# Kernel tuning notes

Hardware: AMD Instinct MI355X
Metric: run time of the kernel (lower is better)

## Reference

```python
import jax, jax.numpy as jnp
import numpy as np

H, E, R = 1024, 48, 32  # hidden size, num entities, num relation types
MAX_START = 200


def setup_inputs() -> dict:
    key = jax.random.key(0)
    ks = jax.random.split(key, 6)
    return {
        "entity_emb": jax.random.normal(ks[0], (E, H), jnp.float32),
        "rel_emb": jax.random.normal(ks[1], (R, H), jnp.float32),
        "W1": jax.random.normal(ks[2], (3 * H, H), jnp.float32) / np.sqrt(3 * H).astype(np.float32),
        "b1": jnp.zeros((H,), jnp.float32),
        "W2": jax.random.normal(ks[3], (H, 1), jnp.float32) / np.sqrt(H).astype(np.float32),
        "b2": jnp.zeros((1,), jnp.float32),
        "entity_starts": jax.random.randint(ks[4], (E,), 0, MAX_START, jnp.int32),
        "max_distance": 50,
    }


def reference(entity_emb, rel_emb, W1, b1, W2, b2, entity_starts, max_distance):
    """Vectorized equivalent of the triple loop: for every (subj i, obj j, rel k)
    score = sigmoid(MLP(cat([subj, rel, obj]))), masked by i != j and
    |start_i - start_j| <= max_distance. Dropout is identity at eval."""
    e, h = entity_emb.shape
    r = rel_emb.shape[0]
    # build all triplet inputs [E, E, R, 3H] (cat order: subject, relation, object)
    s = jnp.broadcast_to(entity_emb[:, None, None, :], (e, e, r, h))
    rel = jnp.broadcast_to(rel_emb[None, None, :, :], (e, e, r, h))
    o = jnp.broadcast_to(entity_emb[None, :, None, :], (e, e, r, h))
    trip = jnp.concatenate([s, rel, o], axis=-1)  # [E, E, R, 3H]
    hid = jax.nn.relu(jnp.einsum("sorf,fh->sorh", trip, W1) + b1)  # [E, E, R, H]
    logits = jnp.einsum("sorh,hx->sorx", hid, W2)[..., 0] + b2[0]  # [E, E, R]
    scores = jax.nn.sigmoid(logits)
    # pair mask: no self-relations, distance cutoff
    dist = jnp.abs(entity_starts[:, None] - entity_starts[None, :])
    mask = (dist <= max_distance) & (~jnp.eye(e, dtype=bool))  # [E, E]
    return jnp.where(mask[:, :, None], scores, jnp.zeros((), scores.dtype))
```

## Files before the change

kernel.cpp:

```cpp
#include <hip/hip_runtime.h>
#include <hip/hip_bf16.h>
#include <math.h>

#define Hh 1024
#define Ee 48
#define Rr 32
#define PITCH_A 1028
#define PITCH_B 516

union F4 { float4 v; float f[4]; };

__global__ __launch_bounds__(512) void kA_table(const float* __restrict__ ent,
                                                const float* __restrict__ rel,
                                                const float* __restrict__ W1,
                                                const float* __restrict__ b1,
                                                float* __restrict__ T) {
    __shared__ float se[16 * PITCH_A];
    const int tid = threadIdx.x;
    const int rt = blockIdx.x & 7;
    const int h0 = (blockIdx.x >> 3) * 32;
    const int row0 = rt * 16;

    const float* emb; int foff;
    if (row0 < 48)      { emb = ent + row0 * Hh;        foff = 0;      }
    else if (row0 < 80) { emb = rel + (row0 - 48) * Hh; foff = Hh;     }
    else                { emb = ent + (row0 - 80) * Hh; foff = 2 * Hh; }

    for (int q = 0; q < 8; ++q) {
        const int id4 = tid + q * 512;
        const int r = id4 >> 8, o4 = id4 & 255;
        *reinterpret_cast<float4*>(&se[r * PITCH_A + o4 * 4]) =
            *reinterpret_cast<const float4*>(&emb[r * Hh + o4 * 4]);
    }
    __syncthreads();

    const int w    = tid >> 6;
    const int lane = tid & 63;
    const int h4g  = lane & 7;
    const int rsub = lane >> 3;
    const int r0 = rsub * 2, r1 = r0 + 1;
    const int fb = w * 128;

    const float* w1p = W1 + (size_t)(foff + fb) * Hh + h0 + h4g * 4;
    const float* e0p = se + r0 * PITCH_A + fb;
    const float* e1p = se + r1 * PITCH_A + fb;

    float acc[2][4];
#pragma unroll
    for (int a = 0; a < 2; ++a)
#pragma unroll
        for (int c = 0; c < 4; ++c) acc[a][c] = 0.f;

    F4 wk[4];
#pragma unroll
    for (int c = 0; c < 4; ++c)
        wk[c].v = *reinterpret_cast<const float4*>(w1p + (size_t)c * Hh);

    for (int s = 0; s < 32; ++s) {
        const int f = s * 4;
        F4 wn[4];
        if (s < 31) {
#pragma unroll
            for (int c = 0; c < 4; ++c)
                wn[c].v = *reinterpret_cast<const float4*>(w1p + (size_t)(f + 4 + c) * Hh);
        }
        F4 e0, e1;
        e0.v = *reinterpret_cast<const float4*>(e0p + f);
        e1.v = *reinterpret_cast<const float4*>(e1p + f);
#pragma unroll
        for (int c = 0; c < 4; ++c) {
#pragma unroll
            for (int hh = 0; hh < 4; ++hh) {
                acc[0][hh] = fmaf(e0.f[c], wk[c].f[hh], acc[0][hh]);
                acc[1][hh] = fmaf(e1.f[c], wk[c].f[hh], acc[1][hh]);
            }
        }
        if (s < 31) {
#pragma unroll
            for (int c = 0; c < 4; ++c) wk[c] = wn[c];
        }
    }

    __syncthreads();
    {
        float* part = se;
        const int base = (w * 64 + lane) * 8;
        F4 o0, o1;
#pragma unroll
        for (int c = 0; c < 4; ++c) { o0.f[c] = acc[0][c]; o1.f[c] = acc[1][c]; }
        *reinterpret_cast<float4*>(&part[base])     = o0.v;
        *reinterpret_cast<float4*>(&part[base + 4]) = o1.v;
    }
    __syncthreads();
    {
        const int r = tid >> 5, h = tid & 31;
        const int src = ((r >> 1) * 8 + (h >> 2)) * 8 + (r & 1) * 4 + (h & 3);
        float s = 0.f;
#pragma unroll
        for (int ww = 0; ww < 8; ++ww) s += se[ww * 512 + src];
        const int row = row0 + r;
        if (row >= 48 && row < 80) s += b1[h0 + h];
        T[row * Hh + h0 + h] = s;
    }
}

__global__ __launch_bounds__(512) void kB_triplets(const float* __restrict__ T,
                                                   const float* __restrict__ W2,
                                                   const float* __restrict__ b2,
                                                   const int* __restrict__ starts,
                                                   const int* __restrict__ maxd,
                                                   float* __restrict__ out) {
    __shared__ float se[42 * PITCH_B];
    const int tid = threadIdx.x;
    const int i  = blockIdx.x >> 2;
    const int js = (blockIdx.x >> 1) & 1;
    const int ks = blockIdx.x & 1;
    const int j0 = js * 24;
    const int k0 = ks * 16;

    const int w    = tid >> 6;
    const int lane = tid & 63;
    const int jG = lane & 7;
    const int kG = lane >> 3;

    float acc[3][2];
#pragma unroll
    for (int a = 0; a < 3; ++a) { acc[a][0] = 0.f; acc[a][1] = 0.f; }

    for (int c = 0; c < 2; ++c) {
        const int hbase = c * 512;
        __syncthreads();
        for (int q = 0; q < 11; ++q) {
            const int id4 = tid + q * 512;
            if (id4 < 5376) {
                const int g = id4 >> 7, o4 = id4 & 127;
                const float* src;
                if (g == 41) src = W2 + hbase + o4 * 4;
                else {
                    int grow;
                    if (g == 0)       grow = i;
                    else if (g < 17)  grow = 48 + k0 + (g - 1);
                    else              grow = 80 + j0 + (g - 17);
                    src = T + grow * Hh + hbase + o4 * 4;
                }
                *reinterpret_cast<float4*>(&se[g * PITCH_B + o4 * 4]) =
                    *reinterpret_cast<const float4*>(src);
            }
        }
        __syncthreads();

        const int hw = w * 64;
        const float* pa = se + hw;
        const float* pw = se + 41 * PITCH_B + hw;

#pragma unroll
        for (int s = 0; s < 16; ++s) {
            const int h4 = s * 4;
            F4 av, wv, rv[2], bv[3];
            av.v = *reinterpret_cast<const float4*>(pa + h4);
            wv.v = *reinterpret_cast<const float4*>(pw + h4);
#pragma unroll
            for (int tk = 0; tk < 2; ++tk)
                rv[tk].v = *reinterpret_cast<const float4*>(se + (1 + kG + 8 * tk) * PITCH_B + hw + h4);
#pragma unroll
            for (int tj = 0; tj < 3; ++tj)
                bv[tj].v = *reinterpret_cast<const float4*>(se + (17 + jG + 8 * tj) * PITCH_B + hw + h4);

#pragma unroll
            for (int cc = 0; cc < 4; ++cc) {
                const float a = av.f[cc], w2v = wv.f[cc];
                const float p0 = a + rv[0].f[cc];
                const float p1 = a + rv[1].f[cc];
#pragma unroll
                for (int tj = 0; tj < 3; ++tj) {
                    const float bb = bv[tj].f[cc];
                    float v0 = p0 + bb; v0 = v0 > 0.f ? v0 : 0.f;
                    acc[tj][0] = fmaf(v0, w2v, acc[tj][0]);
                    float v1 = p1 + bb; v1 = v1 > 0.f ? v1 : 0.f;
                    acc[tj][1] = fmaf(v1, w2v, acc[tj][1]);
                }
            }
        }
    }

    __syncthreads();
    {
        float* part = se;
#pragma unroll
        for (int tj = 0; tj < 3; ++tj)
#pragma unroll
            for (int tk = 0; tk < 2; ++tk)
                part[w * 384 + (tj * 8 + jG) * 16 + tk * 8 + kG] = acc[tj][tk];
    }
    __syncthreads();
    if (tid < 384) {
        float s = b2[0];
#pragma unroll
        for (int ww = 0; ww < 8; ++ww) s += se[ww * 384 + tid];
        const int jl = tid >> 4, kl = tid & 15;
        const int j = j0 + jl, k = k0 + kl;
        const float sc = 1.f / (1.f + expf(-s));
        int di = starts[i] - starts[j]; if (di < 0) di = -di;
        const bool m = (i != j) && (di <= maxd[0]);
        out[(i * Ee + j) * Rr + k] = m ? sc : 0.f;
    }
}

extern "C" void kernel_launch(void* const* d_in, const int* in_sizes, int n_in,
                              void* d_out, int out_size, void* d_ws, size_t ws_size,
                              hipStream_t stream) {
    const float* ent    = (const float*)d_in[0];
    const float* rel    = (const float*)d_in[1];
    const float* W1     = (const float*)d_in[2];
    const float* b1     = (const float*)d_in[3];
    const float* W2     = (const float*)d_in[4];
    const float* b2     = (const float*)d_in[5];
    const int*   starts = (const int*)d_in[6];
    const int*   maxd   = (const int*)d_in[7];
    float* out = (float*)d_out;

    float* T = (float*)d_ws;

    kA_table<<<256, 512, 0, stream>>>(ent, rel, W1, b1, T);
    kB_triplets<<<192, 512, 0, stream>>>(T, W2, b2, starts, maxd, out);
}
```

Baseline: 29.34 us.

## Double-buffer W1 and T tiles through LDS in both kernels

The table kernel now stages W1 in 256-row chunks into a double-buffered shared-memory tile, transposed so each h-group reads contiguous weights, instead of streaming W1 from global memory straight into registers. The triplet kernel splits the hidden dimension into four 256-wide chunks with ping-pong LDS buffers, so the global loads for the next chunk are issued before computing on the current one. The goal is to overlap global loads with FMA work and hide latency. In exchange, LDS use grows (kA goes to about 130KB), which may limit occupancy, and there are more barriers.

```diff
diff --git a/kernel.cpp b/kernel.cpp
--- a/kernel.cpp
+++ b/kernel.cpp
@@ -6,7 +6,10 @@
 #define Ee 48
 #define Rr 32
 #define PITCH_A 1028
-#define PITCH_B 516
+#define GP_A 1028
+#define BKa 256
+#define PITCH_B 260
+#define CH_B 256
 
 union F4 { float4 v; float f[4]; };
 
@@ -15,7 +18,8 @@
                                                 const float* __restrict__ W1,
                                                 const float* __restrict__ b1,
                                                 float* __restrict__ T) {
-    __shared__ float se[16 * PITCH_A];
+    __shared__ float emb_s[16 * PITCH_A];
+    __shared__ float w_s[2][8 * GP_A];
     const int tid = threadIdx.x;
     const int rt = blockIdx.x & 7;
     const int h0 = (blockIdx.x >> 3) * 32;
@@ -29,67 +33,70 @@
     for (int q = 0; q < 8; ++q) {
         const int id4 = tid + q * 512;
         const int r = id4 >> 8, o4 = id4 & 255;
-        *reinterpret_cast<float4*>(&se[r * PITCH_A + o4 * 4]) =
+        *reinterpret_cast<float4*>(&emb_s[r * PITCH_A + o4 * 4]) =
             *reinterpret_cast<const float4*>(&emb[r * Hh + o4 * 4]);
     }
-    __syncthreads();
 
     const int w    = tid >> 6;
     const int lane = tid & 63;
     const int h4g  = lane & 7;
     const int rsub = lane >> 3;
-    const int r0 = rsub * 2, r1 = r0 + 1;
-    const int fb = w * 128;
-
-    const float* w1p = W1 + (size_t)(foff + fb) * Hh + h0 + h4g * 4;
-    const float* e0p = se + r0 * PITCH_A + fb;
-    const float* e1p = se + r1 * PITCH_A + fb;
-
-    float acc[2][4];
-#pragma unroll
-    for (int a = 0; a < 2; ++a)
-#pragma unroll
-        for (int c = 0; c < 4; ++c) acc[a][c] = 0.f;
-
-    F4 wk[4];
-#pragma unroll
-    for (int c = 0; c < 4; ++c)
-        wk[c].v = *reinterpret_cast<const float4*>(w1p + (size_t)c * Hh);
-
-    for (int s = 0; s < 32; ++s) {
-        const int f = s * 4;
-        F4 wn[4];
-        if (s < 31) {
-#pragma unroll
-            for (int c = 0; c < 4; ++c)
-                wn[c].v = *reinterpret_cast<const float4*>(w1p + (size_t)(f + 4 + c) * Hh);
-        }
-        F4 e0, e1;
-        e0.v = *reinterpret_cast<const float4*>(e0p + f);
-        e1.v = *reinterpret_cast<const float4*>(e1p + f);
-#pragma unroll
-        for (int c = 0; c < 4; ++c) {
-#pragma unroll
-            for (int hh = 0; hh < 4; ++hh) {
-                acc[0][hh] = fmaf(e0.f[c], wk[c].f[hh], acc[0][hh]);
-                acc[1][hh] = fmaf(e1.f[c], wk[c].f[hh], acc[1][hh]);
+    const int r0 = rsub * 2;
+
+    const int sc4 = tid & 7;
+    const int sfb = tid >> 3;
+    auto stage = [&](int buf, int c) {
+        const float* gp = &W1[(size_t)(foff + c * BKa + sfb) * Hh + h0 + sc4 * 4];
+        float4 v0 = *reinterpret_cast<const float4*>(gp);
+        float4 v1 = *reinterpret_cast<const float4*>(gp + (size_t)64 * Hh);
+        float4 v2 = *reinterpret_cast<const float4*>(gp + (size_t)128 * Hh);
+        float4 v3 = *reinterpret_cast<const float4*>(gp + (size_t)192 * Hh);
+        float* lp = &w_s[buf][sc4 * GP_A + sfb * 4];
+        *reinterpret_cast<float4*>(lp)       = v0;
+        *reinterpret_cast<float4*>(lp + 256) = v1;
+        *reinterpret_cast<float4*>(lp + 512) = v2;
+        *reinterpret_cast<float4*>(lp + 768) = v3;
+    };
+
+    stage(0, 0);
+    __syncthreads();
+
+    float acc0[4] = {0.f, 0.f, 0.f, 0.f};
+    float acc1[4] = {0.f, 0.f, 0.f, 0.f};
+
+    for (int c = 0; c < 4; ++c) {
+        if (c < 3) stage((c + 1) & 1, c + 1);
+
+        const float* wp  = &w_s[c & 1][h4g * GP_A + (w * 32) * 4];
+        const float* e0p = &emb_s[r0 * PITCH_A + c * BKa + w * 32];
+        const float* e1p = e0p + PITCH_A;
+
+#pragma unroll
+        for (int s = 0; s < 8; ++s) {
+            F4 e0, e1;
+            e0.v = *reinterpret_cast<const float4*>(e0p + s * 4);
+            e1.v = *reinterpret_cast<const float4*>(e1p + s * 4);
+#pragma unroll
+            for (int ff = 0; ff < 4; ++ff) {
+                F4 wv;
+                wv.v = *reinterpret_cast<const float4*>(wp + (s * 4 + ff) * 4);
+#pragma unroll
+                for (int hh = 0; hh < 4; ++hh) {
+                    acc0[hh] = fmaf(e0.f[ff], wv.f[hh], acc0[hh]);
+                    acc1[hh] = fmaf(e1.f[ff], wv.f[hh], acc1[hh]);
+                }
             }
         }
-        if (s < 31) {
-#pragma unroll
-            for (int c = 0; c < 4; ++c) wk[c] = wn[c];
-        }
-    }
-
-    __syncthreads();
+        __syncthreads();
+    }
+
     {
-        float* part = se;
         const int base = (w * 64 + lane) * 8;
         F4 o0, o1;
 #pragma unroll
-        for (int c = 0; c < 4; ++c) { o0.f[c] = acc[0][c]; o1.f[c] = acc[1][c]; }
-        *reinterpret_cast<float4*>(&part[base])     = o0.v;
-        *reinterpret_cast<float4*>(&part[base + 4]) = o1.v;
+        for (int c = 0; c < 4; ++c) { o0.f[c] = acc0[c]; o1.f[c] = acc1[c]; }
+        *reinterpret_cast<float4*>(&emb_s[base])     = o0.v;
+        *reinterpret_cast<float4*>(&emb_s[base + 4]) = o1.v;
     }
     __syncthreads();
     {
@@ -97,7 +104,7 @@
         const int src = ((r >> 1) * 8 + (h >> 2)) * 8 + (r & 1) * 4 + (h & 3);
         float s = 0.f;
 #pragma unroll
-        for (int ww = 0; ww < 8; ++ww) s += se[ww * 512 + src];
+        for (int ww = 0; ww < 8; ++ww) s += emb_s[ww * 512 + src];
         const int row = row0 + r;
         if (row >= 48 && row < 80) s += b1[h0 + h];
         T[row * Hh + h0 + h] = s;
@@ -110,7 +117,7 @@
                                                    const int* __restrict__ starts,
                                                    const int* __restrict__ maxd,
                                                    float* __restrict__ out) {
-    __shared__ float se[42 * PITCH_B];
+    __shared__ float se[2][42 * PITCH_B];
     const int tid = threadIdx.x;
     const int i  = blockIdx.x >> 2;
     const int js = (blockIdx.x >> 1) & 1;
@@ -123,48 +130,69 @@
     const int jG = lane & 7;
     const int kG = lane >> 3;
 
+    auto stage = [&](int buf, int c) {
+        const int hbase = c * CH_B;
+        float4 v0, v1, v2, v3, v4, v5;
+        int a5 = -1;
+#define SRC_OF(ID4, VV)                                                       \
+        {                                                                     \
+            const int g = (ID4) >> 6, o4 = (ID4) & 63;                        \
+            const float* src;                                                 \
+            if (g == 41) src = W2 + hbase + o4 * 4;                           \
+            else {                                                            \
+                int grow;                                                     \
+                if (g == 0)       grow = i;                                   \
+                else if (g < 17)  grow = 48 + k0 + (g - 1);                   \
+                else              grow = 80 + j0 + (g - 17);                  \
+                src = T + grow * Hh + hbase + o4 * 4;                         \
+            }                                                                 \
+            VV = *reinterpret_cast<const float4*>(src);                       \
+        }
+        SRC_OF(tid,          v0)
+        SRC_OF(tid + 512,    v1)
+        SRC_OF(tid + 1024,   v2)
+        SRC_OF(tid + 1536,   v3)
+        SRC_OF(tid + 2048,   v4)
+        if (tid < 128) { SRC_OF(tid + 2560, v5) a5 = tid + 2560; }
+#undef SRC_OF
+        float* b = se[buf];
+        {
+            const int id4 = tid;        *reinterpret_cast<float4*>(&b[(id4 >> 6) * PITCH_B + (id4 & 63) * 4]) = v0;
+        }
+        { const int id4 = tid + 512;    *reinterpret_cast<float4*>(&b[(id4 >> 6) * PITCH_B + (id4 & 63) * 4]) = v1; }
+        { const int id4 = tid + 1024;   *reinterpret_cast<float4*>(&b[(id4 >> 6) * PITCH_B + (id4 & 63) * 4]) = v2; }
+        { const int id4 = tid + 1536;   *reinterpret_cast<float4*>(&b[(id4 >> 6) * PITCH_B + (id4 & 63) * 4]) = v3; }
+        { const int id4 = tid + 2048;   *reinterpret_cast<float4*>(&b[(id4 >> 6) * PITCH_B + (id4 & 63) * 4]) = v4; }
+        if (a5 >= 0) { *reinterpret_cast<float4*>(&b[(a5 >> 6) * PITCH_B + (a5 & 63) * 4]) = v5; }
+    };
+
+    stage(0, 0);
+    __syncthreads();
+
     float acc[3][2];
 #pragma unroll
     for (int a = 0; a < 3; ++a) { acc[a][0] = 0.f; acc[a][1] = 0.f; }
 
-    for (int c = 0; c < 2; ++c) {
-        const int hbase = c * 512;
-        __syncthreads();
-        for (int q = 0; q < 11; ++q) {
-            const int id4 = tid + q * 512;
-            if (id4 < 5376) {
-                const int g = id4 >> 7, o4 = id4 & 127;
-                const float* src;
-                if (g == 41) src = W2 + hbase + o4 * 4;
-                else {
-                    int grow;
-                    if (g == 0)       grow = i;
-                    else if (g < 17)  grow = 48 + k0 + (g - 1);
-                    else              grow = 80 + j0 + (g - 17);
-                    src = T + grow * Hh + hbase + o4 * 4;
-                }
-                *reinterpret_cast<float4*>(&se[g * PITCH_B + o4 * 4]) =
-                    *reinterpret_cast<const float4*>(src);
-            }
-        }
-        __syncthreads();
-
-        const int hw = w * 64;
-        const float* pa = se + hw;
-        const float* pw = se + 41 * PITCH_B + hw;
-
-#pragma unroll
-        for (int s = 0; s < 16; ++s) {
+    for (int c = 0; c < 4; ++c) {
+        if (c < 3) stage((c + 1) & 1, c + 1);
+
+        const float* sm = se[c & 1];
+        const int hw = w * 32;
+        const float* pa = sm + hw;
+        const float* pw = sm + 41 * PITCH_B + hw;
+
+#pragma unroll
+        for (int s = 0; s < 8; ++s) {
             const int h4 = s * 4;
             F4 av, wv, rv[2], bv[3];
             av.v = *reinterpret_cast<const float4*>(pa + h4);
             wv.v = *reinterpret_cast<const float4*>(pw + h4);
 #pragma unroll
             for (int tk = 0; tk < 2; ++tk)
-                rv[tk].v = *reinterpret_cast<const float4*>(se + (1 + kG + 8 * tk) * PITCH_B + hw + h4);
+                rv[tk].v = *reinterpret_cast<const float4*>(sm + (1 + kG + 8 * tk) * PITCH_B + hw + h4);
 #pragma unroll
             for (int tj = 0; tj < 3; ++tj)
-                bv[tj].v = *reinterpret_cast<const float4*>(se + (17 + jG + 8 * tj) * PITCH_B + hw + h4);
+                bv[tj].v = *reinterpret_cast<const float4*>(sm + (17 + jG + 8 * tj) * PITCH_B + hw + h4);
 
 #pragma unroll
             for (int cc = 0; cc < 4; ++cc) {
@@ -181,22 +209,19 @@
                 }
             }
         }
-    }
-
-    __syncthreads();
-    {
-        float* part = se;
-#pragma unroll
-        for (int tj = 0; tj < 3; ++tj)
-#pragma unroll
-            for (int tk = 0; tk < 2; ++tk)
-                part[w * 384 + (tj * 8 + jG) * 16 + tk * 8 + kG] = acc[tj][tk];
-    }
+        __syncthreads();
+    }
+
+#pragma unroll
+    for (int tj = 0; tj < 3; ++tj)
+#pragma unroll
+        for (int tk = 0; tk < 2; ++tk)
+            se[0][w * 384 + (tj * 8 + jG) * 16 + tk * 8 + kG] = acc[tj][tk];
     __syncthreads();
     if (tid < 384) {
         float s = b2[0];
 #pragma unroll
-        for (int ww = 0; ww < 8; ++ww) s += se[ww * 384 + tid];
+        for (int ww = 0; ww < 8; ++ww) s += se[0][ww * 384 + tid];
         const int jl = tid >> 4, kl = tid & 15;
         const int j = j0 + jl, k = k0 + kl;
         const float sc = 1.f / (1.f + expf(-s));
```

Result: faster. 28.53 us (-2.8%).
